# Kernel tuning notes

Measured on AMD Instinct MI355X. Metric: run time of the kernel, lower is better.

Reference implementation:

```python
import jax, jax.numpy as jnp
import numpy as np

N, Q, E, D = 100000, 128, 500000, 32
D4 = 4 * D
RATIO_UPDATE = 0.2
NEG_SLOPE = 0.01  # LeakyReLU default


def setup_inputs() -> dict:
    key = jax.random.key(0)
    ks = jax.random.split(key, 16)
    return {
        "visited_node_score": jax.random.uniform(ks[0], (N,), jnp.float32),
        "node_repr": jax.random.normal(ks[1], (N, D), jnp.float32),
        "eg0": jnp.sort(jax.random.randint(ks[2], (E,), 0, Q)),
        "src0": jax.random.randint(ks[3], (E,), 0, N),
        "dst0": jax.random.randint(ks[4], (E,), 0, N),
        "rel0": jax.random.normal(ks[5], (E, D), jnp.float32),
        "eg1": jnp.sort(jax.random.randint(ks[6], (E,), 0, Q)),
        "src1": jax.random.randint(ks[7], (E,), 0, N),
        "dst1": jax.random.randint(ks[8], (E,), 0, N),
        "rel1": jax.random.normal(ks[9], (E, D), jnp.float32),
        "query_src_emb": jax.random.normal(ks[10], (Q, D), jnp.float32),
        "query_rel_emb": jax.random.normal(ks[11], (Q, D), jnp.float32),
        "Wq": jax.random.normal(ks[12], (D4, D4), jnp.float32) * np.sqrt(2.0 / D4).astype(np.float32),
        "Wk": jax.random.normal(ks[13], (D4, D4), jnp.float32) * np.sqrt(2.0 / D4).astype(np.float32),
        "Wlin": jax.random.normal(ks[14], (D, D), jnp.float32) * np.sqrt(2.0 / (2 * D)).astype(np.float32),
        "blin": jnp.zeros((D,), jnp.float32),
        "max_edges": 500,
    }


def segment_softmax(logits, seg, num_segments):
    # softmax within groups of identical seg id (source node index)
    m = jax.ops.segment_max(logits, seg, num_segments=num_segments)
    ex = jnp.exp(logits - m[seg])
    s = jax.ops.segment_sum(ex, seg, num_segments=num_segments)
    return ex / s[seg]


def segment_topk_mask(values, seg, k):
    # keep mask for per-segment top-k (seg must be sorted); stable -> first occurrence on ties
    n = values.shape[0]
    order = jnp.lexsort((-values, seg))  # primary: seg, secondary: descending value
    seg_sorted = seg[order]
    idx = jnp.arange(n)
    is_start = jnp.concatenate([jnp.array([True]), seg_sorted[1:] != seg_sorted[:-1]])
    seg_start = jax.lax.cummax(jnp.where(is_start, idx, 0))
    rank_sorted = idx - seg_start  # rank within segment, 0 = largest
    rank = jnp.zeros((n,), jnp.int32).at[order].set(rank_sorted.astype(jnp.int32))
    return rank < k


def reference(visited_node_score, node_repr, eg0, src0, dst0, rel0,
              eg1, src1, dst1, rel1, query_src_emb, query_rel_emb,
              Wq, Wk, Wlin, blin, max_edges):
    def att_logits(repr_, src, dst, eg, rel):
        q = query_src_emb[eg]
        r = query_rel_emb[eg]
        left = jnp.concatenate([repr_[src], rel, q, r], axis=-1)   # [E, 4D]
        right = jnp.concatenate([repr_[dst], rel, q, r], axis=-1)  # [E, 4D]
        return jnp.sum((left @ Wq.T) * (right @ Wk.T), axis=-1)    # [E]

    num_nodes = node_repr.shape[0]

    # ---- last layer: attention + segmented top-k pruning ----
    logits1 = att_logits(node_repr, src1, dst1, eg1, rel1)
    w1 = segment_softmax(logits1, src1, num_nodes)           # softmax over out-edges of each src node
    src_score = visited_node_score[src1]
    target_score = w1 * src_score
    keep = segment_topk_mask(target_score, eg1, max_edges)   # top-k per eg_idx
    w1p = jnp.where(keep, w1, 0.0)

    # node score aggregation == 'sum': score[n] = sum_{kept e: dst=n} w * src_score
    updated_node_score = jax.ops.segment_sum(w1p * src_score, dst1, num_segments=num_nodes)

    # representation update along pruned edges (linear_act=False)
    agg = jax.ops.segment_sum(w1p[:, None] * node_repr[src1], dst1, num_segments=num_nodes)
    repr_ = (1.0 - RATIO_UPDATE) * agg + RATIO_UPDATE * node_repr

    # ---- earlier layer(s), no pruning ----
    logits0 = att_logits(repr_, src0, dst0, eg0, rel0)
    w0 = segment_softmax(logits0, src0, num_nodes)
    agg0 = jax.ops.segment_sum(w0[:, None] * repr_[src0], dst0, num_segments=num_nodes)
    repr_ = (1.0 - RATIO_UPDATE) * agg0 + RATIO_UPDATE * repr_

    # bypass_forward: LeakyReLU(Linear(repr))
    h = repr_ @ Wlin.T + blin
    updated_repr = jnp.where(h >= 0, h, NEG_SLOPE * h)
    return updated_node_score, updated_repr
```

## Files before the change

### kernel.cpp

```cpp
#include <hip/hip_runtime.h>
#include <math.h>

#define DD 32
#define DD4 128
#define TPB 256
#define LDSCAP 6144
#define CANDCAP 2048

__device__ __forceinline__ unsigned long long dsort_key(double x) {
  unsigned long long b = (unsigned long long)__double_as_longlong(x);
  return (b & 0x8000000000000000ull) ? ~b : (b | 0x8000000000000000ull);
}
__device__ __forceinline__ double dunsort_key(unsigned long long k) {
  unsigned long long b = (k & 0x8000000000000000ull) ? (k ^ 0x8000000000000000ull) : ~k;
  return __longlong_as_double((long long)b);
}
__device__ __forceinline__ unsigned int fsort_key(float x) {
  unsigned int b = __float_as_uint(x);
  return (b & 0x80000000u) ? ~b : (b | 0x80000000u);
}
__device__ __forceinline__ float funsort_key(unsigned int k) {
  unsigned int b = (k & 0x80000000u) ? (k ^ 0x80000000u) : ~k;
  return __uint_as_float(b);
}

__device__ __forceinline__ int block_iscan256(int x, int* wsum) {
  const int lane = threadIdx.x & 63, w = threadIdx.x >> 6;
#pragma unroll
  for (int o = 1; o < 64; o <<= 1) {
    int y = __shfl_up(x, o, 64);
    if (lane >= o) x += y;
  }
  if (lane == 63) wsum[w] = x;
  __syncthreads();
  int add = 0;
#pragma unroll
  for (int i = 0; i < 4; ++i) add += (i < w) ? wsum[i] : 0;
  __syncthreads();
  return x + add;
}

__global__ __launch_bounds__(TPB) void k_precompute_M(
    const float* __restrict__ Wq, const float* __restrict__ Wk,
    double* __restrict__ M64, float* __restrict__ M32) {
  int t = blockIdx.x * blockDim.x + threadIdx.x;
  int i = t >> 7, j = t & 127;
  double acc = 0.0;
  for (int k = 0; k < DD4; ++k)
    acc += (double)Wq[k * DD4 + i] * (double)Wk[k * DD4 + j];
  M64[i * DD4 + j] = acc;
  M32[i * DD4 + j] = (float)acc;
}

__global__ __launch_bounds__(TPB) void k_sym22(
    const double* __restrict__ M64, double* __restrict__ S64, float* __restrict__ S32) {
  int i = blockIdx.x * blockDim.x + threadIdx.x;
  int r = i >> 5, c = i & 31;
  double g  = M64[(32 + r) * DD4 + 32 + c];
  double gt = M64[(32 + c) * DD4 + 32 + r];
  double s = (c > r) ? (g + gt) : ((c == r) ? g : 0.0);
  S64[i] = s;
  S32[i] = (float)s;
}

__global__ __launch_bounds__(64) void k_per_query(
    const double* __restrict__ M64,
    const float* __restrict__ qemb, const float* __restrict__ remb,
    double* __restrict__ p64, double* __restrict__ pD64, double* __restrict__ c64,
    float* __restrict__ p32, float* __restrict__ pD32, float* __restrict__ c32) {
  int q = blockIdx.x;
  int l = threadIdx.x;
  __shared__ double qr[64];
  qr[l] = (l < DD) ? (double)qemb[q * DD + l] : (double)remb[q * DD + (l - DD)];
  __syncthreads();
  double a = 0.0;
  for (int j = 0; j < 64; ++j) a += M64[l * DD4 + 64 + j] * qr[j];
  double ct = 0.0;
  for (int j = 0; j < 64; ++j) ct += M64[(64 + j) * DD4 + l] * qr[j];
  if (l >= DD) a += ct;
  p64[q * 64 + l] = a;
  p32[q * 64 + l] = (float)a;
  if (l < DD) {
    pD64[q * DD + l] = ct;
    pD32[q * DD + l] = (float)ct;
  }
  double a3 = 0.0;
  for (int j = 0; j < 64; ++j) a3 += M64[(64 + l) * DD4 + 64 + j] * qr[j];
  a3 *= qr[l];
  for (int o = 32; o; o >>= 1) a3 += __shfl_xor(a3, o);
  if (l == 0) { c64[q] = a3; c32[q] = (float)a3; }
}

#define G_T(c) Mmat[(c) * DD4 + j]
#define G_U(c) Mmat[j * DD4 + 32 + (c)]
#define G_V(c) Mmat[(32 + (c)) * DD4 + j]

#define NP_TILE(GEXPR)                                                          \
  for (int tt = 0; tt < 4; ++tt) {                                              \
    T a0=(T)0,a1=(T)0,a2=(T)0,a3=(T)0,a4=(T)0,a5=(T)0,a6=(T)0,a7=(T)0;          \
    const int c0 = tt * 8;                                                      \
    _Pragma("unroll")                                                           \
    for (int j = 0; j < 32; ++j) {                                              \
      const T hj = hh[j];                                                       \
      a0 += (GEXPR(c0 + 0)) * hj; a1 += (GEXPR(c0 + 1)) * hj;                   \
      a2 += (GEXPR(c0 + 2)) * hj; a3 += (GEXPR(c0 + 3)) * hj;                   \
      a4 += (GEXPR(c0 + 4)) * hj; a5 += (GEXPR(c0 + 5)) * hj;                   \
      a6 += (GEXPR(c0 + 6)) * hj; a7 += (GEXPR(c0 + 7)) * hj;                   \
    }                                                                           \
    xq[tid * 9 + tt * 2]     = make_float4((float)a0,(float)a1,(float)a2,(float)a3); \
    xq[tid * 9 + tt * 2 + 1] = make_float4((float)a4,(float)a5,(float)a6,(float)a7); \
  }

#define NP_STORE(dst)                                                           \
  __syncthreads();                                                              \
  {                                                                             \
    float4* go = (float4*)(dst) + (size_t)nbase * 8;                            \
    _Pragma("unroll")                                                           \
    for (int k = 0; k < 8; ++k) {                                               \
      int f = k * TPB + tid;                                                    \
      if ((f >> 3) < nlim) go[f] = xq[(f >> 3) * 9 + (f & 7)];                  \
    }                                                                           \
  }                                                                             \
  __syncthreads();

template <typename T, bool MIX>
__global__ __launch_bounds__(TPB) void k_node_pre(
    const T* __restrict__ Mmat, const float* __restrict__ reprIn,
    const float* __restrict__ aggIn, float* __restrict__ reprOut,
    float* __restrict__ t, float* __restrict__ u, float* __restrict__ v, int N_) {
  __shared__ float xp[TPB * 36];
  float4* xq = (float4*)xp;
  const int tid = threadIdx.x;
  const int nbase = blockIdx.x * TPB;
  const int n = nbase + tid;
  const int nlim = min(TPB, N_ - nbase);
  const bool valid = tid < nlim;
  T hh[32];
  if (valid) {
    const float4* h4 = (const float4*)reprIn + (size_t)n * 8;
#pragma unroll
    for (int jq = 0; jq < 8; ++jq) {
      float4 x = h4[jq];
      if constexpr (MIX) {
        const float4 a = ((const float4*)aggIn)[(size_t)n * 8 + jq];
        x = make_float4(0.8f * a.x + 0.2f * x.x, 0.8f * a.y + 0.2f * x.y,
                        0.8f * a.z + 0.2f * x.z, 0.8f * a.w + 0.2f * x.w);
        xq[tid * 9 + jq] = x;
      }
      hh[4 * jq]     = (T)x.x; hh[4 * jq + 1] = (T)x.y;
      hh[4 * jq + 2] = (T)x.z; hh[4 * jq + 3] = (T)x.w;
    }
  } else {
#pragma unroll
    for (int j = 0; j < 32; ++j) hh[j] = (T)0;
  }
  if constexpr (MIX) {
    NP_STORE(reprOut)
  }
  NP_TILE(G_T)
  NP_STORE(t)
  NP_TILE(G_U)
  NP_STORE(u)
  NP_TILE(G_V)
  NP_STORE(v)
}

template <typename T>
__global__ __launch_bounds__(TPB) void k_quad(
    const T* __restrict__ Smat,
    const float* __restrict__ rel, const int* __restrict__ eg,
    const T* __restrict__ pq, const T* __restrict__ cq,
    T* __restrict__ quad, int E) {
  const int e = blockIdx.x * TPB + threadIdx.x;
  if (e >= E) return;
  const int q = eg[e];
  T rl[32];
  {
    const float4* r4 = (const float4*)rel + (size_t)e * 8;
#pragma unroll
    for (int j = 0; j < 8; ++j) {
      float4 x = r4[j];
      rl[4 * j] = (T)x.x; rl[4 * j + 1] = (T)x.y;
      rl[4 * j + 2] = (T)x.z; rl[4 * j + 3] = (T)x.w;
    }
  }
  const T* prow = pq + (size_t)q * 64 + 32;
  T lin0 = (T)0, lin1 = (T)0;
#pragma unroll
  for (int i = 0; i < 32; i += 2) {
    lin0 += prow[i] * rl[i];
    lin1 += prow[i + 1] * rl[i + 1];
  }
  T a0 = cq[q] + lin0, a1 = lin1, a2 = (T)0, a3 = (T)0;
#pragma unroll
  for (int i = 0; i < 32; ++i) {
    T r0 = Smat[i * 32 + i] * rl[i];
    T r1 = (T)0;
#pragma unroll
    for (int j = i + 1; j < 32; ++j) {
      if ((j - i) & 1) r1 += Smat[i * 32 + j] * rl[j];
      else             r0 += Smat[i * 32 + j] * rl[j];
    }
    T rr = (r0 + r1) * rl[i];
    if ((i & 3) == 0) a0 += rr;
    else if ((i & 3) == 1) a1 += rr;
    else if ((i & 3) == 2) a2 += rr;
    else a3 += rr;
  }
  quad[e] = (a0 + a1) + (a2 + a3);
}

template <typename T>
__global__ __launch_bounds__(TPB) void k_edge_dots(
    const float* __restrict__ repr, const float* __restrict__ rel,
    const int* __restrict__ src, const int* __restrict__ dst, const int* __restrict__ eg,
    const float* __restrict__ tvec, const float* __restrict__ uvec, const float* __restrict__ vvec,
    const T* __restrict__ pq, const T* __restrict__ pDq, const T* __restrict__ quad,
    T* __restrict__ logits, void* __restrict__ mkey, int E) {
  const long long t = (long long)blockIdx.x * TPB + threadIdx.x;
  const int e = (int)(t >> 3), part = (int)(t & 7);
  if (e >= E) return;
  const int s = src[e], d = dst[e], q = eg[e];
  const float4 hs = ((const float4*)repr)[(size_t)s * 8 + part];
  const float4 td = ((const float4*)tvec)[(size_t)d * 8 + part];
  const float4 hd = ((const float4*)repr)[(size_t)d * 8 + part];
  const float4 rl = ((const float4*)rel)[(size_t)e * 8 + part];
  const float4 us = ((const float4*)uvec)[(size_t)s * 8 + part];
  const float4 vd = ((const float4*)vvec)[(size_t)d * 8 + part];
  const T* p  = pq  + (size_t)q * 64 + part * 4;
  const T* pD = pDq + (size_t)q * DD + part * 4;
  T a = (T)hs.x * ((T)td.x + p[0]) + (T)hs.y * ((T)td.y + p[1]) +
        (T)hs.z * ((T)td.z + p[2]) + (T)hs.w * ((T)td.w + p[3]);
  a += (T)hd.x * pD[0] + (T)hd.y * pD[1] + (T)hd.z * pD[2] + (T)hd.w * pD[3];
  a += (T)rl.x * (T)(us.x + vd.x) + (T)rl.y * (T)(us.y + vd.y) +
       (T)rl.z * (T)(us.z + vd.z) + (T)rl.w * (T)(us.w + vd.w);
  a += __shfl_xor(a, 1);
  a += __shfl_xor(a, 2);
  a += __shfl_xor(a, 4);
  if (part == 0) {
    a += quad[e];
    logits[e] = a;
    if constexpr (sizeof(T) == 8) {
      atomicMax((unsigned long long*)mkey + s, dsort_key((double)a));
    } else {
      atomicMax((unsigned int*)mkey + s, fsort_key((float)a));
    }
  }
}

__global__ __launch_bounds__(TPB) void k_expsum64(
    double* __restrict__ io, const unsigned long long* __restrict__ mkey,
    const int* __restrict__ src, double* __restrict__ ssum, int E) {
  int e = blockIdx.x * blockDim.x + threadIdx.x;
  if (e >= E) return;
  int s = src[e];
  double ex = exp(io[e] - dunsort_key(mkey[s]));
  io[e] = ex;
  atomicAdd(&ssum[s], ex);
}
__global__ __launch_bounds__(TPB) void k_expsum32h(
    float* __restrict__ io, const unsigned int* __restrict__ mkey,
    const int* __restrict__ src, const int* __restrict__ dst,
    float* __restrict__ ssum, int* __restrict__ cnt, int E) {
  int e = blockIdx.x * blockDim.x + threadIdx.x;
  if (e >= E) return;
  int s = src[e];
  float ex = expf(io[e] - funsort_key(mkey[s]));
  io[e] = ex;
  atomicAdd(&ssum[s], ex);
  atomicAdd(&cnt[dst[e]], 1);
}

__global__ __launch_bounds__(TPB) void k_weights_target(
    const double* __restrict__ ex, const double* __restrict__ ssum,
    const int* __restrict__ src, const float* __restrict__ score,
    const int* __restrict__ eg, int* __restrict__ qoff,
    float* __restrict__ w1f, unsigned int* __restrict__ tkey, int E, int Q) {
  int e = blockIdx.x * blockDim.x + threadIdx.x;
  if (e >= E) return;
  int s = src[e];
  double w = ex[e] / ssum[s];
  float wf = (float)w;
  w1f[e] = wf;
  float tgt = wf * score[s];
  tkey[e] = fsort_key(tgt);
  int cur = eg[e];
  int prev = (e == 0) ? -1 : eg[e - 1];
  for (int v = prev + 1; v <= cur; ++v) qoff[v] = e;
  if (e == E - 1) {
    for (int v = cur + 1; v <= Q; ++v) qoff[v] = E;
  }
}

__global__ __launch_bounds__(TPB) void k_topk(
    const unsigned int* __restrict__ tkey, const float* __restrict__ w1f,
    const int* __restrict__ qoff, const int* __restrict__ maxe,
    float* __restrict__ w1p, int E) {
  __shared__ unsigned int keys[LDSCAP];
  __shared__ int hist[256];
  __shared__ unsigned short cand[CANDCAP];
  __shared__ int wsum[4];
  __shared__ int sh_cnt;
  __shared__ unsigned int sh_prefix;
  __shared__ int sh_need;
  const int q = blockIdx.x;
  const int s = qoff[q], e2 = qoff[q + 1];
  const int n = e2 - s;
  const int K = maxe[0];
  if (n <= K) {
    for (int i = s + threadIdx.x; i < e2; i += TPB) w1p[i] = w1f[i];
    return;
  }
  const bool useLds = (n <= LDSCAP);
  if (useLds) {
    for (int i = threadIdx.x; i < n; i += TPB) keys[i] = tkey[s + i];
  }
  hist[threadIdx.x] = 0;
  __syncthreads();
  for (int i = threadIdx.x; i < n; i += TPB) {
    unsigned int k = useLds ? keys[i] : tkey[s + i];
    atomicAdd(&hist[k >> 24], 1);
  }
  __syncthreads();
  int need = K;
  {
    int h = hist[255 - threadIdx.x];
    int incl = block_iscan256(h, wsum);
    int excl = incl - h;
    if (incl >= need && excl < need) {
      sh_prefix = (unsigned int)(255 - threadIdx.x) << 24;
      sh_need = need - excl;
    }
  }
  __syncthreads();
  unsigned int prefix = sh_prefix;
  need = sh_need;
  const int cnt0 = hist[prefix >> 24];
  const bool compact = useLds && (cnt0 <= CANDCAP);
  if (threadIdx.x == 0) sh_cnt = 0;
  __syncthreads();
  if (compact) {
    const unsigned int d0 = prefix >> 24;
    for (int i = threadIdx.x; i < n; i += TPB) {
      if ((keys[i] >> 24) == d0) {
        int p = atomicAdd(&sh_cnt, 1);
        cand[p] = (unsigned short)i;
      }
    }
  }
  __syncthreads();
  const int ncand = compact ? sh_cnt : 0;
  for (int pass = 1; pass < 4; ++pass) {
    const int shift = 24 - 8 * pass;
    const unsigned int himask = 0xFFFFFFFFu << (shift + 8);
    hist[threadIdx.x] = 0;
    __syncthreads();
    if (compact) {
      for (int ci = threadIdx.x; ci < ncand; ci += TPB) {
        unsigned int k = keys[cand[ci]];
        if ((k & himask) == prefix) atomicAdd(&hist[(k >> shift) & 255], 1);
      }
    } else {
      for (int i = threadIdx.x; i < n; i += TPB) {
        unsigned int k = useLds ? keys[i] : tkey[s + i];
        if ((k & himask) == prefix) atomicAdd(&hist[(k >> shift) & 255], 1);
      }
    }
    __syncthreads();
    int h = hist[255 - threadIdx.x];
    int incl = block_iscan256(h, wsum);
    int excl = incl - h;
    if (incl >= need && excl < need) {
      sh_prefix = prefix | ((unsigned int)(255 - threadIdx.x) << shift);
      sh_need = need - excl;
    }
    __syncthreads();
    prefix = sh_prefix;
    need = sh_need;
    __syncthreads();
  }
  const unsigned int kth = prefix;
  const int r = need;
  const int C = (n + TPB - 1) / TPB;
  const int b0 = min(threadIdx.x * C, n);
  const int b1 = min(b0 + C, n);
  int myt = 0;
  for (int i = b0; i < b1; ++i) {
    unsigned int k = useLds ? keys[i] : tkey[s + i];
    myt += (k == kth) ? 1 : 0;
  }
  int tincl = block_iscan256(myt, wsum);
  int tiepre = tincl - myt;
  for (int i = b0; i < b1; ++i) {
    unsigned int k = useLds ? keys[i] : tkey[s + i];
    float v = 0.f;
    if (k > kth) {
      v = w1f[s + i];
    } else if (k == kth) {
      if (tiepre < r) v = w1f[s + i];
      ++tiepre;
    }
    w1p[s + i] = v;
  }
}

__global__ __launch_bounds__(TPB) void k_apply1(
    const float* __restrict__ w1p, const int* __restrict__ src, const int* __restrict__ dst,
    const float* __restrict__ repr0, const float* __restrict__ score,
    float* __restrict__ agg, float* __restrict__ score_out, int E) {
  int t = blockIdx.x * blockDim.x + threadIdx.x;
  int e = t >> 3, part = t & 7;
  if (e >= E) return;
  float w = w1p[e];
  if (w == 0.f) return;
  int sv = src[e], dv = dst[e];
  const float4 rv = ((const float4*)repr0)[sv * 8 + part];
  float* ap = agg + (size_t)dv * DD + part * 4;
  atomicAdd(ap + 0, w * rv.x);
  atomicAdd(ap + 1, w * rv.y);
  atomicAdd(ap + 2, w * rv.z);
  atomicAdd(ap + 3, w * rv.w);
  if (part == 0) atomicAdd(score_out + dv, w * score[sv]);
}

#define SCHUNK 1024
__global__ __launch_bounds__(TPB) void k_scan1(
    const int* __restrict__ cnt, int* __restrict__ off, int* __restrict__ bsum, int N_) {
  __shared__ int sd[TPB];
  const int b = blockIdx.x, t = threadIdx.x;
  const int base = b * SCHUNK + t * 4;
  int v[4];
  int s4 = 0;
#pragma unroll
  for (int k = 0; k < 4; ++k) {
    v[k] = (base + k < N_) ? cnt[base + k] : 0;
    s4 += v[k];
  }
  sd[t] = s4;
  __syncthreads();
  for (int o = 1; o < TPB; o <<= 1) {
    int x = (t >= o) ? sd[t - o] : 0;
    __syncthreads();
    sd[t] += x;
    __syncthreads();
  }
  int excl = sd[t] - s4;
  if (t == TPB - 1) bsum[b] = sd[t];
  int run = excl;
#pragma unroll
  for (int k = 0; k < 4; ++k) {
    if (base + k < N_) { off[base + k] = run; run += v[k]; }
  }
}

__global__ __launch_bounds__(TPB) void k_scan2(
    int* __restrict__ bsum, int* __restrict__ off, int nblk, int N_, int E) {
  __shared__ int wsum[4];
  if (nblk <= TPB) {
    int t = threadIdx.x;
    int x = (t < nblk) ? bsum[t] : 0;
    int orig = x;
    const int lane = t & 63, w = t >> 6;
#pragma unroll
    for (int o = 1; o < 64; o <<= 1) {
      int y = __shfl_up(x, o, 64);
      if (lane >= o) x += y;
    }
    if (lane == 63) wsum[w] = x;
    __syncthreads();
    int add = 0;
#pragma unroll
    for (int i = 0; i < 4; ++i) add += (i < w) ? wsum[i] : 0;
    x += add;
    if (t < nblk) bsum[t] = x - orig;
    if (t == 0) off[N_] = E;
  } else {
    if (threadIdx.x != 0) return;
    int run = 0;
    for (int i = 0; i < nblk; ++i) { int tmp = bsum[i]; bsum[i] = run; run += tmp; }
    off[N_] = E;
  }
}

__global__ __launch_bounds__(TPB) void k_scan3(
    int* __restrict__ off, const int* __restrict__ bsum, int* __restrict__ cursor, int N_) {
  int i = blockIdx.x * blockDim.x + threadIdx.x;
  if (i >= N_) return;
  int v = off[i] + bsum[i >> 10];
  off[i] = v;
  cursor[i] = v;
}

__global__ __launch_bounds__(TPB) void k_scatter0(
    const float* __restrict__ ex, const float* __restrict__ ssum,
    const int* __restrict__ src, const int* __restrict__ dst,
    int* __restrict__ cursor, float2* __restrict__ pk, int E) {
  int e = blockIdx.x * blockDim.x + threadIdx.x;
  if (e >= E) return;
  int s = src[e];
  float w = ex[e] / ssum[s];
  int pos = atomicAdd(&cursor[dst[e]], 1);
  pk[pos] = make_float2(w, __int_as_float(s));
}

__global__ __launch_bounds__(TPB) void k_gather_mix(
    const float2* __restrict__ pk, const int* __restrict__ off,
    const float* __restrict__ repr1, float* __restrict__ mixbuf, int N_) {
  const int n = blockIdx.x * 8 + (threadIdx.x >> 5);
  const int c = threadIdx.x & 31;
  if (n >= N_) return;
  const float self = repr1[(size_t)n * DD + c];
  float acc = 0.f;
  const int j0 = off[n], j1 = off[n + 1];
  int j = j0;
  for (; j + 4 <= j1; j += 4) {
    const float2 p0 = pk[j], p1 = pk[j + 1], p2 = pk[j + 2], p3 = pk[j + 3];
    const float g0 = repr1[(size_t)__float_as_int(p0.y) * DD + c];
    const float g1 = repr1[(size_t)__float_as_int(p1.y) * DD + c];
    const float g2 = repr1[(size_t)__float_as_int(p2.y) * DD + c];
    const float g3 = repr1[(size_t)__float_as_int(p3.y) * DD + c];
    acc += p0.x * g0;
    acc += p1.x * g1;
    acc += p2.x * g2;
    acc += p3.x * g3;
  }
  for (; j < j1; ++j) {
    const float2 p = pk[j];
    acc += p.x * repr1[(size_t)__float_as_int(p.y) * DD + c];
  }
  mixbuf[(size_t)n * DD + c] = 0.8f * acc + 0.2f * self;
}

__global__ __launch_bounds__(TPB) void k_final_linear(
    const float* __restrict__ Wlin, const float* __restrict__ blin,
    const float* __restrict__ mixbuf, float* __restrict__ out_repr, int N_) {
  __shared__ float xp[TPB * 36];
  float4* xq = (float4*)xp;
  const int tid = threadIdx.x;
  const int nbase = blockIdx.x * TPB;
  const int n = nbase + tid;
  const int nlim = min(TPB, N_ - nbase);
  float m[32];
  if (tid < nlim) {
    const float4* h4 = (const float4*)mixbuf + (size_t)n * 8;
#pragma unroll
    for (int jq = 0; jq < 8; ++jq) {
      float4 x = h4[jq];
      m[4 * jq] = x.x; m[4 * jq + 1] = x.y; m[4 * jq + 2] = x.z; m[4 * jq + 3] = x.w;
    }
  } else {
#pragma unroll
    for (int j = 0; j < 32; ++j) m[j] = 0.f;
  }
  for (int tt = 0; tt < 4; ++tt) {
    const int c0 = tt * 8;
    float a0 = blin[c0 + 0], a1 = blin[c0 + 1], a2 = blin[c0 + 2], a3 = blin[c0 + 3];
    float a4 = blin[c0 + 4], a5 = blin[c0 + 5], a6 = blin[c0 + 6], a7 = blin[c0 + 7];
#pragma unroll
    for (int j = 0; j < 32; ++j) {
      const float hj = m[j];
      a0 += Wlin[(c0 + 0) * DD + j] * hj; a1 += Wlin[(c0 + 1) * DD + j] * hj;
      a2 += Wlin[(c0 + 2) * DD + j] * hj; a3 += Wlin[(c0 + 3) * DD + j] * hj;
      a4 += Wlin[(c0 + 4) * DD + j] * hj; a5 += Wlin[(c0 + 5) * DD + j] * hj;
      a6 += Wlin[(c0 + 6) * DD + j] * hj; a7 += Wlin[(c0 + 7) * DD + j] * hj;
    }
    a0 = (a0 >= 0.f) ? a0 : 0.01f * a0; a1 = (a1 >= 0.f) ? a1 : 0.01f * a1;
    a2 = (a2 >= 0.f) ? a2 : 0.01f * a2; a3 = (a3 >= 0.f) ? a3 : 0.01f * a3;
    a4 = (a4 >= 0.f) ? a4 : 0.01f * a4; a5 = (a5 >= 0.f) ? a5 : 0.01f * a5;
    a6 = (a6 >= 0.f) ? a6 : 0.01f * a6; a7 = (a7 >= 0.f) ? a7 : 0.01f * a7;
    xq[tid * 9 + tt * 2]     = make_float4(a0, a1, a2, a3);
    xq[tid * 9 + tt * 2 + 1] = make_float4(a4, a5, a6, a7);
  }
  NP_STORE(out_repr)
}

extern "C" void kernel_launch(void* const* d_in, const int* in_sizes, int n_in,
                              void* d_out, int out_size, void* d_ws, size_t ws_size,
                              hipStream_t stream) {
  (void)n_in; (void)out_size; (void)ws_size;
  const float* score = (const float*)d_in[0];
  const float* nrepr = (const float*)d_in[1];
  const int*   eg0   = (const int*)d_in[2];
  const int*   src0  = (const int*)d_in[3];
  const int*   dst0  = (const int*)d_in[4];
  const float* rel0  = (const float*)d_in[5];
  const int*   eg1   = (const int*)d_in[6];
  const int*   src1  = (const int*)d_in[7];
  const int*   dst1  = (const int*)d_in[8];
  const float* rel1  = (const float*)d_in[9];
  const float* qemb  = (const float*)d_in[10];
  const float* remb  = (const float*)d_in[11];
  const float* Wq    = (const float*)d_in[12];
  const float* Wk    = (const float*)d_in[13];
  const float* Wlin  = (const float*)d_in[14];
  const float* blin  = (const float*)d_in[15];
  const int*   maxe  = (const int*)d_in[16];

  const int N_ = in_sizes[0];
  const int E_ = in_sizes[2];
  const int Q_ = in_sizes[10] / DD;

  char* wsc = (char*)d_ws;
  size_t off = 0;
  auto alloc = [&](size_t bytes) -> void* {
    void* p = wsc + off;
    off += (bytes + 255) & ~(size_t)255;
    return p;
  };
  double* M64  = (double*)alloc((size_t)DD4 * DD4 * 8);
  float*  M32  = (float*)alloc((size_t)DD4 * DD4 * 4);
  double* S64  = (double*)alloc((size_t)DD * DD * 8);
  float*  S32  = (float*)alloc((size_t)DD * DD * 4);
  double* p64  = (double*)alloc((size_t)Q_ * 64 * 8);
  double* pD64 = (double*)alloc((size_t)Q_ * DD * 8);
  double* c64  = (double*)alloc((size_t)Q_ * 8);
  float*  p32  = (float*)alloc((size_t)Q_ * 64 * 4);
  float*  pD32 = (float*)alloc((size_t)Q_ * DD * 4);
  float*  c32  = (float*)alloc((size_t)Q_ * 4);
  int*    qoff = (int*)alloc((size_t)(Q_ + 2) * 4);
  double* lg1  = (double*)alloc((size_t)E_ * 8);
  double* qv64 = (double*)alloc((size_t)E_ * 8);
  float*  w1f  = (float*)alloc((size_t)E_ * 4);
  unsigned int* tkey = (unsigned int*)alloc((size_t)E_ * 4);
  float*  w1p  = (float*)alloc((size_t)E_ * 4);
  float*  lg0  = (float*)alloc((size_t)E_ * 4);
  float*  repr1 = (float*)alloc((size_t)N_ * DD * 4);
  float*  tvec = (float*)alloc((size_t)N_ * DD * 4);
  float*  uvec = (float*)alloc((size_t)N_ * DD * 4);
  float*  vvec = (float*)alloc((size_t)N_ * DD * 4);
  size_t zstart = off;
  unsigned long long* mkey1 = (unsigned long long*)alloc((size_t)N_ * 8);
  double* s1   = (double*)alloc((size_t)N_ * 8);
  float*  agg  = (float*)alloc((size_t)N_ * DD * 4);
  unsigned int* mkey0 = (unsigned int*)alloc((size_t)N_ * 4);
  float*  s0   = (float*)alloc((size_t)N_ * 4);
  size_t zlen = off - zstart;

  float* qv32 = (float*)qv64;

  int* cnt    = (int*)tvec;
  int* offcsr = (int*)tvec + N_;
  int* cursor = (int*)tvec + 2 * (size_t)N_ + 64;
  int* bsum   = (int*)tvec + 3 * (size_t)N_ + 128;
  float2* pk  = (float2*)uvec;
  float* mixbuf = vvec;

  float* out_score = (float*)d_out;
  float* out_repr  = out_score + N_;

  hipMemsetAsync(wsc + zstart, 0, zlen, stream);
  hipMemsetAsync(d_out, 0, (size_t)N_ * 4, stream);

  k_precompute_M<<<(DD4 * DD4) / TPB, TPB, 0, stream>>>(Wq, Wk, M64, M32);
  k_sym22<<<4, TPB, 0, stream>>>(M64, S64, S32);
  k_per_query<<<Q_, 64, 0, stream>>>(M64, qemb, remb, p64, pD64, c64, p32, pD32, c32);

  const int ngrid = (N_ + TPB - 1) / TPB;
  const int egrid = (E_ + TPB - 1) / TPB;
  const int dgrid = (int)(((size_t)E_ * 8 + TPB - 1) / TPB);

  k_node_pre<double, false><<<ngrid, TPB, 0, stream>>>(M64, nrepr, nullptr, nullptr,
                                                       tvec, uvec, vvec, N_);
  k_quad<double><<<egrid, TPB, 0, stream>>>(S64, rel1, eg1, p64, c64, qv64, E_);
  k_edge_dots<double><<<dgrid, TPB, 0, stream>>>(nrepr, rel1, src1, dst1, eg1,
                                                 tvec, uvec, vvec, p64, pD64, qv64,
                                                 lg1, (void*)mkey1, E_);
  k_expsum64<<<egrid, TPB, 0, stream>>>(lg1, mkey1, src1, s1, E_);
  k_weights_target<<<egrid, TPB, 0, stream>>>(lg1, s1, src1, score, eg1, qoff,
                                              w1f, tkey, E_, Q_);
  k_topk<<<Q_, TPB, 0, stream>>>(tkey, w1f, qoff, maxe, w1p, E_);

  k_apply1<<<dgrid, TPB, 0, stream>>>(w1p, src1, dst1, nrepr, score, agg, out_score, E_);

  k_node_pre<float, true><<<ngrid, TPB, 0, stream>>>(M32, nrepr, agg, repr1,
                                                     tvec, uvec, vvec, N_);
  k_quad<float><<<egrid, TPB, 0, stream>>>(S32, rel0, eg0, p32, c32, qv32, E_);
  k_edge_dots<float><<<dgrid, TPB, 0, stream>>>(repr1, rel0, src0, dst0, eg0,
                                                tvec, uvec, vvec, p32, pD32, qv32,
                                                lg0, (void*)mkey0, E_);

  hipMemsetAsync(cnt, 0, (size_t)N_ * 4, stream);
  k_expsum32h<<<egrid, TPB, 0, stream>>>(lg0, mkey0, src0, dst0, s0, cnt, E_);
  const int nblk = (N_ + SCHUNK - 1) / SCHUNK;
  k_scan1<<<nblk, TPB, 0, stream>>>(cnt, offcsr, bsum, N_);
  k_scan2<<<1, TPB, 0, stream>>>(bsum, offcsr, nblk, N_, E_);
  k_scan3<<<ngrid, TPB, 0, stream>>>(offcsr, bsum, cursor, N_);
  k_scatter0<<<egrid, TPB, 0, stream>>>(lg0, s0, src0, dst0, cursor, pk, E_);
  k_gather_mix<<<(N_ + 7) / 8, TPB, 0, stream>>>(pk, offcsr, repr1, mixbuf, N_);
  k_final_linear<<<ngrid, TPB, 0, stream>>>(Wlin, blin, mixbuf, out_repr, N_);
}
```

Before: 623.6 us.

## Interleave per-node vectors into source and destination records for edge gathers

The node precompute kernel now writes two interleaved per-node arrays. One is a source record holding repr and u (64 floats), the other a destination record holding t, repr and v (96 floats). The edge dot kernel therefore gathers from two contiguous rows per edge instead of six separate arrays. This is meant to improve locality of the random gathers, fetching fewer distinct cache lines and DRAM pages per edge. In exchange, repr is written twice, the workspace grows, and scratch aliases for the later CSR and mix buffers are re-pointed into the new arrays.

```diff
diff --git a/kernel.cpp b/kernel.cpp
--- a/kernel.cpp
+++ b/kernel.cpp
@@ -111,14 +111,16 @@
     xq[tid * 9 + tt * 2 + 1] = make_float4((float)a4,(float)a5,(float)a6,(float)a7); \
   }
 
-#define NP_STORE(dst)                                                           \
+#define NP_STORE(dst, STRIDE4, OFFS4)                                           \
   __syncthreads();                                                              \
   {                                                                             \
-    float4* go = (float4*)(dst) + (size_t)nbase * 8;                            \
+    float4* go = (float4*)(dst) + (size_t)nbase * (STRIDE4);                    \
     _Pragma("unroll")                                                           \
     for (int k = 0; k < 8; ++k) {                                               \
       int f = k * TPB + tid;                                                    \
-      if ((f >> 3) < nlim) go[f] = xq[(f >> 3) * 9 + (f & 7)];                  \
+      if ((f >> 3) < nlim)                                                      \
+        go[(size_t)(f >> 3) * (STRIDE4) + (OFFS4) + (f & 7)] =                  \
+            xq[(f >> 3) * 9 + (f & 7)];                                         \
     }                                                                           \
   }                                                                             \
   __syncthreads();
@@ -127,7 +129,7 @@
 __global__ __launch_bounds__(TPB) void k_node_pre(
     const T* __restrict__ Mmat, const float* __restrict__ reprIn,
     const float* __restrict__ aggIn, float* __restrict__ reprOut,
-    float* __restrict__ t, float* __restrict__ u, float* __restrict__ v, int N_) {
+    float* __restrict__ sn, float* __restrict__ dn, int N_) {
   __shared__ float xp[TPB * 36];
   float4* xq = (float4*)xp;
   const int tid = threadIdx.x;
@@ -145,8 +147,8 @@
         const float4 a = ((const float4*)aggIn)[(size_t)n * 8 + jq];
         x = make_float4(0.8f * a.x + 0.2f * x.x, 0.8f * a.y + 0.2f * x.y,
                         0.8f * a.z + 0.2f * x.z, 0.8f * a.w + 0.2f * x.w);
-        xq[tid * 9 + jq] = x;
       }
+      xq[tid * 9 + jq] = x;
       hh[4 * jq]     = (T)x.x; hh[4 * jq + 1] = (T)x.y;
       hh[4 * jq + 2] = (T)x.z; hh[4 * jq + 3] = (T)x.w;
     }
@@ -155,14 +157,16 @@
     for (int j = 0; j < 32; ++j) hh[j] = (T)0;
   }
   if constexpr (MIX) {
-    NP_STORE(reprOut)
-  }
+    NP_STORE(reprOut, 8, 0)
+  }
+  NP_STORE(sn, 16, 0)
+  NP_STORE(dn, 24, 8)
   NP_TILE(G_T)
-  NP_STORE(t)
+  NP_STORE(dn, 24, 0)
   NP_TILE(G_U)
-  NP_STORE(u)
+  NP_STORE(sn, 16, 8)
   NP_TILE(G_V)
-  NP_STORE(v)
+  NP_STORE(dn, 24, 16)
 }
 
 template <typename T>
@@ -212,21 +216,23 @@
 
 template <typename T>
 __global__ __launch_bounds__(TPB) void k_edge_dots(
-    const float* __restrict__ repr, const float* __restrict__ rel,
+    const float* __restrict__ sn, const float* __restrict__ dn,
+    const float* __restrict__ rel,
     const int* __restrict__ src, const int* __restrict__ dst, const int* __restrict__ eg,
-    const float* __restrict__ tvec, const float* __restrict__ uvec, const float* __restrict__ vvec,
     const T* __restrict__ pq, const T* __restrict__ pDq, const T* __restrict__ quad,
     T* __restrict__ logits, void* __restrict__ mkey, int E) {
   const long long t = (long long)blockIdx.x * TPB + threadIdx.x;
   const int e = (int)(t >> 3), part = (int)(t & 7);
   if (e >= E) return;
   const int s = src[e], d = dst[e], q = eg[e];
-  const float4 hs = ((const float4*)repr)[(size_t)s * 8 + part];
-  const float4 td = ((const float4*)tvec)[(size_t)d * 8 + part];
-  const float4 hd = ((const float4*)repr)[(size_t)d * 8 + part];
+  const float4* sn4 = (const float4*)sn + (size_t)s * 16;
+  const float4* dn4 = (const float4*)dn + (size_t)d * 24;
+  const float4 hs = sn4[part];
+  const float4 us = sn4[8 + part];
+  const float4 td = dn4[part];
+  const float4 hd = dn4[8 + part];
+  const float4 vd = dn4[16 + part];
   const float4 rl = ((const float4*)rel)[(size_t)e * 8 + part];
-  const float4 us = ((const float4*)uvec)[(size_t)s * 8 + part];
-  const float4 vd = ((const float4*)vvec)[(size_t)d * 8 + part];
   const T* p  = pq  + (size_t)q * 64 + part * 4;
   const T* pD = pDq + (size_t)q * DD + part * 4;
   T a = (T)hs.x * ((T)td.x + p[0]) + (T)hs.y * ((T)td.y + p[1]) +
@@ -571,7 +577,7 @@
     xq[tid * 9 + tt * 2]     = make_float4(a0, a1, a2, a3);
     xq[tid * 9 + tt * 2 + 1] = make_float4(a4, a5, a6, a7);
   }
-  NP_STORE(out_repr)
+  NP_STORE(out_repr, 8, 0)
 }
 
 extern "C" void kernel_launch(void* const* d_in, const int* in_sizes, int n_in,
@@ -625,9 +631,8 @@
   float*  w1p  = (float*)alloc((size_t)E_ * 4);
   float*  lg0  = (float*)alloc((size_t)E_ * 4);
   float*  repr1 = (float*)alloc((size_t)N_ * DD * 4);
-  float*  tvec = (float*)alloc((size_t)N_ * DD * 4);
-  float*  uvec = (float*)alloc((size_t)N_ * DD * 4);
-  float*  vvec = (float*)alloc((size_t)N_ * DD * 4);
+  float*  sn   = (float*)alloc((size_t)N_ * 64 * 4);
+  float*  dn   = (float*)alloc((size_t)N_ * 96 * 4);
   size_t zstart = off;
   unsigned long long* mkey1 = (unsigned long long*)alloc((size_t)N_ * 8);
   double* s1   = (double*)alloc((size_t)N_ * 8);
@@ -638,12 +643,12 @@
 
   float* qv32 = (float*)qv64;
 
-  int* cnt    = (int*)tvec;
-  int* offcsr = (int*)tvec + N_;
-  int* cursor = (int*)tvec + 2 * (size_t)N_ + 64;
-  int* bsum   = (int*)tvec + 3 * (size_t)N_ + 128;
-  float2* pk  = (float2*)uvec;
-  float* mixbuf = vvec;
+  int* cnt    = (int*)sn;
+  int* offcsr = (int*)sn + N_;
+  int* cursor = (int*)sn + 2 * (size_t)N_ + 64;
+  int* bsum   = (int*)sn + 3 * (size_t)N_ + 128;
+  float2* pk  = (float2*)dn;
+  float* mixbuf = dn + 2 * (size_t)E_ + 64;
 
   float* out_score = (float*)d_out;
   float* out_repr  = out_score + N_;
@@ -660,10 +665,10 @@
   const int dgrid = (int)(((size_t)E_ * 8 + TPB - 1) / TPB);
 
   k_node_pre<double, false><<<ngrid, TPB, 0, stream>>>(M64, nrepr, nullptr, nullptr,
-                                                       tvec, uvec, vvec, N_);
+                                                       sn, dn, N_);
   k_quad<double><<<egrid, TPB, 0, stream>>>(S64, rel1, eg1, p64, c64, qv64, E_);
-  k_edge_dots<double><<<dgrid, TPB, 0, stream>>>(nrepr, rel1, src1, dst1, eg1,
-                                                 tvec, uvec, vvec, p64, pD64, qv64,
+  k_edge_dots<double><<<dgrid, TPB, 0, stream>>>(sn, dn, rel1, src1, dst1, eg1,
+                                                 p64, pD64, qv64,
                                                  lg1, (void*)mkey1, E_);
   k_expsum64<<<egrid, TPB, 0, stream>>>(lg1, mkey1, src1, s1, E_);
   k_weights_target<<<egrid, TPB, 0, stream>>>(lg1, s1, src1, score, eg1, qoff,
@@ -673,10 +678,10 @@
   k_apply1<<<dgrid, TPB, 0, stream>>>(w1p, src1, dst1, nrepr, score, agg, out_score, E_);
 
   k_node_pre<float, true><<<ngrid, TPB, 0, stream>>>(M32, nrepr, agg, repr1,
-                                                     tvec, uvec, vvec, N_);
+                                                     sn, dn, N_);
   k_quad<float><<<egrid, TPB, 0, stream>>>(S32, rel0, eg0, p32, c32, qv32, E_);
-  k_edge_dots<float><<<dgrid, TPB, 0, stream>>>(repr1, rel0, src0, dst0, eg0,
-                                                tvec, uvec, vvec, p32, pD32, qv32,
+  k_edge_dots<float><<<dgrid, TPB, 0, stream>>>(sn, dn, rel0, src0, dst0, eg0,
+                                                p32, pD32, qv32,
                                                 lg0, (void*)mkey0, E_);
 
   hipMemsetAsync(cnt, 0, (size_t)N_ * 4, stream);
```

Measured after the change: 630.8 us. Within noise of the previous version (+1.2%).
